# Performance work log

Hardware: AMD Instinct MI355X
Metric: run time of the kernel (lower is better)

Reference implementation:

```python
import jax, jax.numpy as jnp
import numpy as np

D_MODEL = 1024
H = 16
D = D_MODEL // H  # 64 per-head dim
B, T = 2, 2048


def setup_inputs() -> dict:
    key = jax.random.key(0)
    ks = jax.random.split(key, 5)
    scale = 1.0 / np.sqrt(D_MODEL)
    x = jax.random.normal(ks[0], (B, T, D_MODEL), dtype=jnp.float32)
    Wqkv = jax.random.normal(ks[1], (D_MODEL, 3 * D_MODEL), dtype=jnp.float32) * scale
    bqkv = jnp.zeros((3 * D_MODEL,), dtype=jnp.float32)
    Wproj = jax.random.normal(ks[2], (D_MODEL, D_MODEL), dtype=jnp.float32) * scale
    bproj = jnp.zeros((D_MODEL,), dtype=jnp.float32)
    return {"x": x, "Wqkv": Wqkv, "bqkv": bqkv, "Wproj": Wproj, "bproj": bproj}


def reference(x, Wqkv, bqkv, Wproj, bproj):
    b, t, d_model = x.shape
    h, d = H, D
    qkv = x @ Wqkv + bqkv  # [b, t, 3*d_model]
    q, k, v = jnp.split(qkv, 3, axis=-1)
    # [b, t, d_model] -> [b, h, t, d]
    q = q.reshape(b, t, h, d).transpose(0, 2, 1, 3)
    k = k.reshape(b, t, h, d).transpose(0, 2, 1, 3)
    v = v.reshape(b, t, h, d).transpose(0, 2, 1, 3)
    att = jnp.einsum('bhqd,bhkd->bhqk', q, k) / jnp.sqrt(jnp.float32(d))
    causal = jnp.tril(jnp.ones((t, t), dtype=bool))  # [t, t]
    att = jnp.where(causal[None, None, :, :], att, -jnp.inf)
    att = jax.nn.softmax(att, axis=-1)
    # dropout in eval mode -> identity (deterministic reference)
    out = jnp.einsum('bhqk,bhkd->bhqd', att, v)  # [b, h, t, d]
    out = out.transpose(0, 2, 1, 3).reshape(b, t, d_model)
    out = out @ Wproj + bproj
    return out
```

## Files before the change

### kernel.cpp

```cpp
#include <hip/hip_runtime.h>
#include <cstddef>

typedef __bf16 bf16x8 __attribute__((ext_vector_type(8)));
typedef float  f32x4  __attribute__((ext_vector_type(4)));

__device__ __forceinline__ float bf2f(unsigned short s) {
    return __uint_as_float(((unsigned int)s) << 16);
}
__device__ __forceinline__ unsigned short f2bf(float x) {
    unsigned int u = __float_as_uint(x);
    unsigned int r = u + 0x7fffu + ((u >> 16) & 1u);
    return (unsigned short)(r >> 16);
}

__device__ __forceinline__ void async_load16(const void* g, void* l) {
    __builtin_amdgcn_global_load_lds(
        (const __attribute__((address_space(1))) unsigned int*)g,
        (__attribute__((address_space(3))) unsigned int*)l,
        16, 0, 0);
}

__global__ __launch_bounds__(256) void detect_dtype_kernel(
    const unsigned short* __restrict__ x, int* __restrict__ flag)
{
    __shared__ int cnt;
    if (threadIdx.x == 0) cnt = 0;
    __syncthreads();
    int wild = 0;
    for (int k = 0; k < 16; ++k) {
        unsigned short u = x[(size_t)((k * 256 + threadIdx.x) << 1)];
        int e = (u >> 7) & 0xFF;
        wild += ((e >= 0x90) || (e >= 1 && e <= 0x48)) ? 1 : 0;
    }
    atomicAdd(&cnt, wild);
    __syncthreads();
    if (threadIdx.x == 0) *flag = (cnt > 512) ? 1 : 0;
}

__global__ __launch_bounds__(256) void cast_kernel(
    const int* __restrict__ flag, const void* __restrict__ src,
    unsigned short* __restrict__ dst, int n8)
{
    const int i = blockIdx.x * 256 + threadIdx.x;
    if (i >= n8) return;
    const size_t off = (size_t)i * 8;
    if (*flag) {
        const float* s = (const float*)src + off;
        float4 a = *(const float4*)s;
        float4 b = *(const float4*)(s + 4);
        uint4 o;
        o.x = (unsigned)f2bf(a.x) | ((unsigned)f2bf(a.y) << 16);
        o.y = (unsigned)f2bf(a.z) | ((unsigned)f2bf(a.w) << 16);
        o.z = (unsigned)f2bf(b.x) | ((unsigned)f2bf(b.y) << 16);
        o.w = (unsigned)f2bf(b.z) | ((unsigned)f2bf(b.w) << 16);
        *(uint4*)(dst + off) = o;
    } else {
        *(uint4*)(dst + off) = *(const uint4*)((const unsigned short*)src + off);
    }
}

__global__ __launch_bounds__(256) void transpose_cast_kernel(
    const int* __restrict__ flag, const void* __restrict__ src,
    unsigned short* __restrict__ dst, int R, int C)
{
    __shared__ unsigned short T[64][72];
    const int c0 = blockIdx.x * 64, r0 = blockIdx.y * 64;
    const int t  = threadIdx.x;
    const int r  = t >> 2, cl = (t & 3) << 4;

    unsigned short v[16];
    if (*flag) {
        const float* s = (const float*)src + (size_t)(r0 + r) * C + c0 + cl;
        #pragma unroll
        for (int q = 0; q < 4; ++q) {
            float4 a = *(const float4*)(s + q * 4);
            v[q * 4 + 0] = f2bf(a.x); v[q * 4 + 1] = f2bf(a.y);
            v[q * 4 + 2] = f2bf(a.z); v[q * 4 + 3] = f2bf(a.w);
        }
    } else {
        const unsigned short* s = (const unsigned short*)src + (size_t)(r0 + r) * C + c0 + cl;
        uint4 a = *(const uint4*)s;
        uint4 b = *(const uint4*)(s + 8);
        unsigned int w[8] = {a.x, a.y, a.z, a.w, b.x, b.y, b.z, b.w};
        #pragma unroll
        for (int q = 0; q < 8; ++q) {
            v[q * 2]     = (unsigned short)(w[q] & 0xffffu);
            v[q * 2 + 1] = (unsigned short)(w[q] >> 16);
        }
    }
    #pragma unroll
    for (int c = 0; c < 16; ++c) T[cl + c][r] = v[c];
    __syncthreads();

    const int c = t >> 2, rl = (t & 3) << 4;
    uint4 o0 = *(const uint4*)&T[c][rl];
    uint4 o1 = *(const uint4*)&T[c][rl + 8];
    unsigned short* dp = dst + (size_t)(c0 + c) * R + r0 + rl;
    *(uint4*)dp       = o0;
    *(uint4*)(dp + 8) = o1;
}

__device__ __forceinline__ void bt_mainloop(
    const unsigned short* __restrict__ A,
    const unsigned short* __restrict__ BT,
    int K, int m0, int n0,
    unsigned short* As, unsigned short* Bs,
    f32x4 (&acc)[4][4])
{
    const int tid  = threadIdx.x;
    const int wave = tid >> 6;
    const int lane = tid & 63;
    const int mrow = lane & 15;
    const int quad = lane >> 4;
    const int wr = wave >> 1, wc = wave & 1;
    const int srow = tid >> 2;
    const int scol = (tid & 3) << 3;

    const unsigned short* ga  = A  + (size_t)(m0 + srow) * K + scol;
    const unsigned short* ga2 = ga + (size_t)64 * K;
    const unsigned short* gb  = BT + (size_t)(n0 + srow) * K + scol;
    const unsigned short* gb2 = gb + (size_t)64 * K;
    unsigned short* lA  = As + wave * 512;
    unsigned short* lA2 = As + 2048 + wave * 512;
    unsigned short* lB  = Bs + wave * 512;
    unsigned short* lB2 = Bs + 2048 + wave * 512;

    for (int k0 = 0; k0 < K; k0 += 32) {
        async_load16(ga,  lA);
        async_load16(ga2, lA2);
        async_load16(gb,  lB);
        async_load16(gb2, lB2);
        ga += 32; ga2 += 32; gb += 32; gb2 += 32;
        __syncthreads();

        bf16x8 afr[4], bfr[4];
        #pragma unroll
        for (int mt = 0; mt < 4; ++mt)
            afr[mt] = *(const bf16x8*)(As + (wr * 64 + mt * 16 + mrow) * 32 + quad * 8);
        #pragma unroll
        for (int nt = 0; nt < 4; ++nt)
            bfr[nt] = *(const bf16x8*)(Bs + (wc * 64 + nt * 16 + mrow) * 32 + quad * 8);
        #pragma unroll
        for (int mt = 0; mt < 4; ++mt) {
            #pragma unroll
            for (int nt = 0; nt < 4; ++nt)
                acc[mt][nt] = __builtin_amdgcn_mfma_f32_16x16x32_bf16(
                    afr[mt], bfr[nt], acc[mt][nt], 0, 0, 0);
        }
        __syncthreads();
    }
}

__global__ __launch_bounds__(256) void gemm_qkv_bt(
    const int* __restrict__ flag,
    const unsigned short* __restrict__ A,
    const unsigned short* __restrict__ BT,
    const void* __restrict__ bias,
    unsigned short* __restrict__ Qb, unsigned short* __restrict__ Kb,
    unsigned short* __restrict__ Vb)
{
    __shared__ unsigned short As[128 * 32];
    __shared__ unsigned short Bs[128 * 32];
    const int m0 = blockIdx.y * 128, n0 = blockIdx.x * 128;

    f32x4 acc[4][4];
    #pragma unroll
    for (int mt = 0; mt < 4; ++mt)
        #pragma unroll
        for (int nt = 0; nt < 4; ++nt)
            { acc[mt][nt][0]=0.f; acc[mt][nt][1]=0.f; acc[mt][nt][2]=0.f; acc[mt][nt][3]=0.f; }

    bt_mainloop(A, BT, 1024, m0, n0, As, Bs, acc);

    const int tid  = threadIdx.x;
    const int wave = tid >> 6;
    const int lane = tid & 63;
    const int mrow = lane & 15;
    const int quad = lane >> 4;
    const int wr = wave >> 1, wc = wave & 1;
    const bool f32b = (*flag != 0);

    #pragma unroll
    for (int nt = 0; nt < 4; ++nt) {
        const int n = n0 + wc * 64 + nt * 16 + mrow;
        const float bv = f32b ? ((const float*)bias)[n]
                              : bf2f(((const unsigned short*)bias)[n]);
        const int sel = n >> 10;
        const int h   = (n & 1023) >> 6;
        const int d   = n & 63;
        unsigned short* dst = (sel == 0) ? Qb : (sel == 1) ? Kb : Vb;
        const float sc = (sel == 0) ? 0.125f : 1.0f;
        #pragma unroll
        for (int mt = 0; mt < 4; ++mt) {
            #pragma unroll
            for (int r = 0; r < 4; ++r) {
                const int m  = m0 + wr * 64 + mt * 16 + quad * 4 + r;
                const int bb = m >> 11;
                const int t  = m & 2047;
                dst[(((size_t)(bb * 16 + h) * 2048 + t) << 6) + d] =
                    f2bf((acc[mt][nt][r] + bv) * sc);
            }
        }
    }
}

__global__ __launch_bounds__(256) void gemm_proj_bt(
    const int* __restrict__ flag,
    const unsigned short* __restrict__ A,
    const unsigned short* __restrict__ BT,
    const void* __restrict__ bias, void* __restrict__ Out)
{
    __shared__ unsigned short As[128 * 32];
    __shared__ unsigned short Bs[128 * 32];
    const int m0 = blockIdx.y * 128, n0 = blockIdx.x * 128;

    f32x4 acc[4][4];
    #pragma unroll
    for (int mt = 0; mt < 4; ++mt)
        #pragma unroll
        for (int nt = 0; nt < 4; ++nt)
            { acc[mt][nt][0]=0.f; acc[mt][nt][1]=0.f; acc[mt][nt][2]=0.f; acc[mt][nt][3]=0.f; }

    bt_mainloop(A, BT, 1024, m0, n0, As, Bs, acc);

    const int tid  = threadIdx.x;
    const int wave = tid >> 6;
    const int lane = tid & 63;
    const int mrow = lane & 15;
    const int quad = lane >> 4;
    const int wr = wave >> 1, wc = wave & 1;
    const bool f32b = (*flag != 0);

    #pragma unroll
    for (int nt = 0; nt < 4; ++nt) {
        const int n = n0 + wc * 64 + nt * 16 + mrow;
        const float bv = f32b ? ((const float*)bias)[n]
                              : bf2f(((const unsigned short*)bias)[n]);
        #pragma unroll
        for (int mt = 0; mt < 4; ++mt) {
            #pragma unroll
            for (int r = 0; r < 4; ++r) {
                const int m = m0 + wr * 64 + mt * 16 + quad * 4 + r;
                const float val = acc[mt][nt][r] + bv;
                if (f32b) ((float*)Out)[(size_t)m * 1024 + n] = val;
                else      ((unsigned short*)Out)[(size_t)m * 1024 + n] = f2bf(val);
            }
        }
    }
}

__global__ __launch_bounds__(256) void attn_kernel(
    const unsigned short* __restrict__ Qb,
    const unsigned short* __restrict__ Kb,
    const unsigned short* __restrict__ Vb,
    unsigned short* __restrict__ Attn)
{
    __shared__ unsigned short Ks[128][68];
    __shared__ unsigned short VsT[64][136];
    __shared__ unsigned short Ps[64][136];

    const int tid  = threadIdx.x;
    const int wave = tid >> 6;
    const int lane = tid & 63;
    const int mrow = lane & 15;
    const int quad = lane >> 4;
    const int bh   = blockIdx.y;
    const int b    = bh >> 4, h = bh & 15;

    const int kr = tid >> 1;
    const int kc = (tid & 1) << 5;
    const int j2  = (tid & 63) << 1;
    const int dgA = (tid >> 6) << 3;

    const unsigned short* Qbase = Qb + ((size_t)bh * 2048) * 64;
    const unsigned short* Kbase = Kb + ((size_t)bh * 2048) * 64;
    const unsigned short* Vbase = Vb + ((size_t)bh * 2048) * 64;

    bf16x8 ones;
    #pragma unroll
    for (int e = 0; e < 8; ++e) ones[e] = (__bf16)1.0f;

    for (int half = 0; half < 2; ++half) {
        const int qblk = (half == 0) ? (int)blockIdx.x : (31 - (int)blockIdx.x);
        const int q0   = qblk << 6;
        const int nr   = (qblk >> 1) + 1;

        bf16x8 aq[2];
        {
            const unsigned short* qp = Qbase + (size_t)(q0 + wave * 16 + mrow) * 64 + quad * 8;
            aq[0] = *(const bf16x8*)qp;
            aq[1] = *(const bf16x8*)(qp + 32);
        }

        f32x4 Oa[4];
        #pragma unroll
        for (int dt = 0; dt < 4; ++dt) { Oa[dt][0]=0.f; Oa[dt][1]=0.f; Oa[dt][2]=0.f; Oa[dt][3]=0.f; }
        float m_run[4] = {-1e30f, -1e30f, -1e30f, -1e30f};
        float l_run[4] = {0.f, 0.f, 0.f, 0.f};

        uint4 kreg[4], vreg[4];
        {
            const unsigned short* kp = Kbase + (size_t)kr * 64 + kc;
            kreg[0] = *(const uint4*)kp;       kreg[1] = *(const uint4*)(kp + 8);
            kreg[2] = *(const uint4*)(kp + 16); kreg[3] = *(const uint4*)(kp + 24);
            const unsigned short* vp = Vbase + (size_t)j2 * 64;
            vreg[0] = *(const uint4*)(vp + dgA);      vreg[1] = *(const uint4*)(vp + 64 + dgA);
            vreg[2] = *(const uint4*)(vp + dgA + 32); vreg[3] = *(const uint4*)(vp + 64 + dgA + 32);
        }

        for (int rr = 0; rr < nr; ++rr) {
            const int kt0 = rr << 7;
            __syncthreads();
            {
                *(uint4*)&Ks[kr][kc]      = kreg[0];
                *(uint4*)&Ks[kr][kc + 8]  = kreg[1];
                *(uint4*)&Ks[kr][kc + 16] = kreg[2];
                *(uint4*)&Ks[kr][kc + 24] = kreg[3];
                #pragma unroll
                for (int g = 0; g < 2; ++g) {
                    const int dg = dgA + g * 32;
                    unsigned int aw[4] = {vreg[g*2].x, vreg[g*2].y, vreg[g*2].z, vreg[g*2].w};
                    unsigned int bw[4] = {vreg[g*2+1].x, vreg[g*2+1].y, vreg[g*2+1].z, vreg[g*2+1].w};
                    #pragma unroll
                    for (int c2 = 0; c2 < 4; ++c2) {
                        unsigned int lo = aw[c2], hi = bw[c2];
                        *(unsigned int*)&VsT[dg + 2*c2][j2]     = (lo & 0xffffu) | (hi << 16);
                        *(unsigned int*)&VsT[dg + 2*c2 + 1][j2] = (lo >> 16) | (hi & 0xffff0000u);
                    }
                }
            }
            __syncthreads();

            if (rr + 1 < nr) {
                const int nt0 = (rr + 1) << 7;
                const unsigned short* kp = Kbase + (size_t)(nt0 + kr) * 64 + kc;
                kreg[0] = *(const uint4*)kp;        kreg[1] = *(const uint4*)(kp + 8);
                kreg[2] = *(const uint4*)(kp + 16); kreg[3] = *(const uint4*)(kp + 24);
                const unsigned short* vp = Vbase + (size_t)(nt0 + j2) * 64;
                vreg[0] = *(const uint4*)(vp + dgA);      vreg[1] = *(const uint4*)(vp + 64 + dgA);
                vreg[2] = *(const uint4*)(vp + dgA + 32); vreg[3] = *(const uint4*)(vp + 64 + dgA + 32);
            }

            f32x4 sacc[8];
            #pragma unroll
            for (int jt = 0; jt < 8; ++jt) { sacc[jt][0]=0.f; sacc[jt][1]=0.f; sacc[jt][2]=0.f; sacc[jt][3]=0.f; }
            #pragma unroll
            for (int ks = 0; ks < 2; ++ks) {
                #pragma unroll
                for (int jt = 0; jt < 8; ++jt) {
                    bf16x8 bk = *(const bf16x8*)&Ks[jt * 16 + mrow][ks * 32 + quad * 8];
                    sacc[jt] = __builtin_amdgcn_mfma_f32_16x16x32_bf16(aq[ks], bk, sacc[jt], 0, 0, 0);
                }
            }

            if (rr == nr - 1) {
                #pragma unroll
                for (int jt = 0; jt < 8; ++jt) {
                    const int jg = kt0 + jt * 16 + mrow;
                    #pragma unroll
                    for (int r = 0; r < 4; ++r) {
                        if (jg > q0 + wave * 16 + quad * 4 + r) sacc[jt][r] = -1e30f;
                    }
                }
            }

            float mx[4], alpha[4];
            #pragma unroll
            for (int r = 0; r < 4; ++r) {
                mx[r] = fmaxf(fmaxf(fmaxf(sacc[0][r], sacc[1][r]), fmaxf(sacc[2][r], sacc[3][r])),
                              fmaxf(fmaxf(sacc[4][r], sacc[5][r]), fmaxf(sacc[6][r], sacc[7][r])));
            }
            #pragma unroll
            for (int m = 1; m <= 8; m <<= 1) {
                #pragma unroll
                for (int r = 0; r < 4; ++r) mx[r] = fmaxf(mx[r], __shfl_xor(mx[r], m));
            }
            #pragma unroll
            for (int r = 0; r < 4; ++r) {
                const float m_new = fmaxf(m_run[r], mx[r]);
                alpha[r] = __expf(m_run[r] - m_new);
                m_run[r] = m_new;
            }

            #pragma unroll
            for (int jt = 0; jt < 8; ++jt) {
                #pragma unroll
                for (int r = 0; r < 4; ++r) {
                    const float pv = __expf(sacc[jt][r] - m_run[r]);
                    Ps[wave * 16 + quad * 4 + r][jt * 16 + mrow] = f2bf(pv);
                }
            }

            #pragma unroll
            for (int dt = 0; dt < 4; ++dt) {
                #pragma unroll
                for (int r = 0; r < 4; ++r) Oa[dt][r] *= alpha[r];
            }

            __threadfence_block();

            f32x4 lt; lt[0]=0.f; lt[1]=0.f; lt[2]=0.f; lt[3]=0.f;
            #pragma unroll
            for (int ks4 = 0; ks4 < 4; ++ks4) {
                bf16x8 ap = *(const bf16x8*)&Ps[wave * 16 + mrow][ks4 * 32 + quad * 8];
                lt = __builtin_amdgcn_mfma_f32_16x16x32_bf16(ap, ones, lt, 0, 0, 0);
                #pragma unroll
                for (int dt = 0; dt < 4; ++dt) {
                    bf16x8 bv = *(const bf16x8*)&VsT[dt * 16 + mrow][ks4 * 32 + quad * 8];
                    Oa[dt] = __builtin_amdgcn_mfma_f32_16x16x32_bf16(ap, bv, Oa[dt], 0, 0, 0);
                }
            }
            #pragma unroll
            for (int r = 0; r < 4; ++r) l_run[r] = l_run[r] * alpha[r] + lt[r];
        }

        #pragma unroll
        for (int r = 0; r < 4; ++r) {
            const float inv = 1.0f / l_run[r];
            const int t = q0 + wave * 16 + quad * 4 + r;
            const size_t base = ((size_t)(b * 2048 + t)) * 1024 + h * 64;
            #pragma unroll
            for (int dt = 0; dt < 4; ++dt)
                Attn[base + dt * 16 + mrow] = f2bf(Oa[dt][r] * inv);
        }
    }
}

extern "C" void kernel_launch(void* const* d_in, const int* in_sizes, int n_in,
                              void* d_out, int out_size, void* d_ws, size_t ws_size,
                              hipStream_t stream)
{
    const void* x     = d_in[0];
    const void* Wqkv  = d_in[1];
    const void* bqkv  = d_in[2];
    const void* Wproj = d_in[3];
    const void* bproj = d_in[4];

    int* flag = (int*)d_ws;
    unsigned short* ws = (unsigned short*)d_ws;
    unsigned short* xb     = ws + 64;
    unsigned short* shared = xb + 4194304;
    unsigned short* WqkvT  = shared;
    unsigned short* Attn   = shared;
    unsigned short* WprojT = shared + 4194304;
    unsigned short* Qb     = WprojT + 1048576;
    unsigned short* Kb     = Qb + 4194304;
    unsigned short* Vb     = Kb + 4194304;

    detect_dtype_kernel<<<1, 256, 0, stream>>>((const unsigned short*)x, flag);
    cast_kernel<<<2048, 256, 0, stream>>>(flag, x, xb, 524288);
    transpose_cast_kernel<<<dim3(48, 16), 256, 0, stream>>>(flag, Wqkv, WqkvT, 1024, 3072);
    transpose_cast_kernel<<<dim3(16, 16), 256, 0, stream>>>(flag, Wproj, WprojT, 1024, 1024);
    gemm_qkv_bt<<<dim3(24, 32), 256, 0, stream>>>(flag, xb, WqkvT, bqkv, Qb, Kb, Vb);
    attn_kernel<<<dim3(16, 32), 256, 0, stream>>>(Qb, Kb, Vb, Attn);
    gemm_proj_bt<<<dim3(8, 32), 256, 0, stream>>>(flag, Attn, WprojT, bproj, d_out);
}
```

Before: 229.3 us.

## Store V transposed from QKV GEMM and async-load K/V tiles into LDS

```diff
diff --git a/kernel.cpp b/kernel.cpp
--- a/kernel.cpp
+++ b/kernel.cpp
@@ -157,7 +157,7 @@
     const unsigned short* __restrict__ BT,
     const void* __restrict__ bias,
     unsigned short* __restrict__ Qb, unsigned short* __restrict__ Kb,
-    unsigned short* __restrict__ Vb)
+    unsigned short* __restrict__ VbT)
 {
     __shared__ unsigned short As[128 * 32];
     __shared__ unsigned short Bs[128 * 32];
@@ -188,7 +188,6 @@
         const int sel = n >> 10;
         const int h   = (n & 1023) >> 6;
         const int d   = n & 63;
-        unsigned short* dst = (sel == 0) ? Qb : (sel == 1) ? Kb : Vb;
         const float sc = (sel == 0) ? 0.125f : 1.0f;
         #pragma unroll
         for (int mt = 0; mt < 4; ++mt) {
@@ -197,8 +196,11 @@
                 const int m  = m0 + wr * 64 + mt * 16 + quad * 4 + r;
                 const int bb = m >> 11;
                 const int t  = m & 2047;
-                dst[(((size_t)(bb * 16 + h) * 2048 + t) << 6) + d] =
-                    f2bf((acc[mt][nt][r] + bv) * sc);
+                const unsigned short ov = f2bf((acc[mt][nt][r] + bv) * sc);
+                const int bhh = bb * 16 + h;
+                if (sel == 0)      Qb [(((size_t)bhh * 2048 + t) << 6) + d] = ov;
+                else if (sel == 1) Kb [(((size_t)bhh * 2048 + t) << 6) + d] = ov;
+                else               VbT[((((size_t)bhh << 6) + d) << 11) + t] = ov;
             }
         }
     }
@@ -252,11 +254,11 @@
 __global__ __launch_bounds__(256) void attn_kernel(
     const unsigned short* __restrict__ Qb,
     const unsigned short* __restrict__ Kb,
-    const unsigned short* __restrict__ Vb,
+    const unsigned short* __restrict__ VbT,
     unsigned short* __restrict__ Attn)
 {
-    __shared__ unsigned short Ks[128][68];
-    __shared__ unsigned short VsT[64][136];
+    __shared__ unsigned short KsH[2][128 * 32];
+    __shared__ unsigned short VsQ[4][64 * 32];
     __shared__ unsigned short Ps[64][136];
 
     const int tid  = threadIdx.x;
@@ -264,24 +266,27 @@
     const int lane = tid & 63;
     const int mrow = lane & 15;
     const int quad = lane >> 4;
-    const int bh   = blockIdx.y;
-    const int b    = bh >> 4, h = bh & 15;
-
-    const int kr = tid >> 1;
-    const int kc = (tid & 1) << 5;
-    const int j2  = (tid & 63) << 1;
-    const int dgA = (tid >> 6) << 3;
-
-    const unsigned short* Qbase = Qb + ((size_t)bh * 2048) * 64;
-    const unsigned short* Kbase = Kb + ((size_t)bh * 2048) * 64;
-    const unsigned short* Vbase = Vb + ((size_t)bh * 2048) * 64;
+
+    const int blk   = blockIdx.x;
+    const int xcd   = blk & 7;
+    const int slot  = blk >> 3;
+    const int bh    = (xcd << 2) | (slot & 3);
+    const int qpair = slot >> 2;
+    const int b     = bh >> 4, h = bh & 15;
+
+    const int krow  = tid >> 2;
+    const int kcol8 = (tid & 3) << 3;
+
+    const unsigned short* Qbase = Qb  + ((size_t)bh << 17);
+    const unsigned short* Kbase = Kb  + ((size_t)bh << 17);
+    const unsigned short* Vtb   = VbT + ((size_t)bh << 17);
 
     bf16x8 ones;
     #pragma unroll
     for (int e = 0; e < 8; ++e) ones[e] = (__bf16)1.0f;
 
     for (int half = 0; half < 2; ++half) {
-        const int qblk = (half == 0) ? (int)blockIdx.x : (31 - (int)blockIdx.x);
+        const int qblk = (half == 0) ? qpair : (31 - qpair);
         const int q0   = qblk << 6;
         const int nr   = (qblk >> 1) + 1;
 
@@ -298,48 +303,25 @@
         float m_run[4] = {-1e30f, -1e30f, -1e30f, -1e30f};
         float l_run[4] = {0.f, 0.f, 0.f, 0.f};
 
-        uint4 kreg[4], vreg[4];
-        {
-            const unsigned short* kp = Kbase + (size_t)kr * 64 + kc;
-            kreg[0] = *(const uint4*)kp;       kreg[1] = *(const uint4*)(kp + 8);
-            kreg[2] = *(const uint4*)(kp + 16); kreg[3] = *(const uint4*)(kp + 24);
-            const unsigned short* vp = Vbase + (size_t)j2 * 64;
-            vreg[0] = *(const uint4*)(vp + dgA);      vreg[1] = *(const uint4*)(vp + 64 + dgA);
-            vreg[2] = *(const uint4*)(vp + dgA + 32); vreg[3] = *(const uint4*)(vp + 64 + dgA + 32);
-        }
-
         for (int rr = 0; rr < nr; ++rr) {
             const int kt0 = rr << 7;
+
+            #pragma unroll
+            for (int h2 = 0; h2 < 2; ++h2) {
+                #pragma unroll
+                for (int p = 0; p < 2; ++p) {
+                    const unsigned short* src =
+                        Kbase + (size_t)(kt0 + p * 64 + krow) * 64 + h2 * 32 + kcol8;
+                    async_load16(src, &KsH[h2][(p * 64 + krow) * 32 + kcol8]);
+                }
+            }
+            #pragma unroll
+            for (int q4 = 0; q4 < 4; ++q4) {
+                const unsigned short* src =
+                    Vtb + ((size_t)krow << 11) + kt0 + q4 * 32 + kcol8;
+                async_load16(src, &VsQ[q4][krow * 32 + kcol8]);
+            }
             __syncthreads();
-            {
-                *(uint4*)&Ks[kr][kc]      = kreg[0];
-                *(uint4*)&Ks[kr][kc + 8]  = kreg[1];
-                *(uint4*)&Ks[kr][kc + 16] = kreg[2];
-                *(uint4*)&Ks[kr][kc + 24] = kreg[3];
-                #pragma unroll
-                for (int g = 0; g < 2; ++g) {
-                    const int dg = dgA + g * 32;
-                    unsigned int aw[4] = {vreg[g*2].x, vreg[g*2].y, vreg[g*2].z, vreg[g*2].w};
-                    unsigned int bw[4] = {vreg[g*2+1].x, vreg[g*2+1].y, vreg[g*2+1].z, vreg[g*2+1].w};
-                    #pragma unroll
-                    for (int c2 = 0; c2 < 4; ++c2) {
-                        unsigned int lo = aw[c2], hi = bw[c2];
-                        *(unsigned int*)&VsT[dg + 2*c2][j2]     = (lo & 0xffffu) | (hi << 16);
-                        *(unsigned int*)&VsT[dg + 2*c2 + 1][j2] = (lo >> 16) | (hi & 0xffff0000u);
-                    }
-                }
-            }
-            __syncthreads();
-
-            if (rr + 1 < nr) {
-                const int nt0 = (rr + 1) << 7;
-                const unsigned short* kp = Kbase + (size_t)(nt0 + kr) * 64 + kc;
-                kreg[0] = *(const uint4*)kp;        kreg[1] = *(const uint4*)(kp + 8);
-                kreg[2] = *(const uint4*)(kp + 16); kreg[3] = *(const uint4*)(kp + 24);
-                const unsigned short* vp = Vbase + (size_t)(nt0 + j2) * 64;
-                vreg[0] = *(const uint4*)(vp + dgA);      vreg[1] = *(const uint4*)(vp + 64 + dgA);
-                vreg[2] = *(const uint4*)(vp + dgA + 32); vreg[3] = *(const uint4*)(vp + 64 + dgA + 32);
-            }
 
             f32x4 sacc[8];
             #pragma unroll
@@ -348,7 +330,7 @@
             for (int ks = 0; ks < 2; ++ks) {
                 #pragma unroll
                 for (int jt = 0; jt < 8; ++jt) {
-                    bf16x8 bk = *(const bf16x8*)&Ks[jt * 16 + mrow][ks * 32 + quad * 8];
+                    bf16x8 bk = *(const bf16x8*)&KsH[ks][(jt * 16 + mrow) * 32 + quad * 8];
                     sacc[jt] = __builtin_amdgcn_mfma_f32_16x16x32_bf16(aq[ks], bk, sacc[jt], 0, 0, 0);
                 }
             }
@@ -406,12 +388,14 @@
                 lt = __builtin_amdgcn_mfma_f32_16x16x32_bf16(ap, ones, lt, 0, 0, 0);
                 #pragma unroll
                 for (int dt = 0; dt < 4; ++dt) {
-                    bf16x8 bv = *(const bf16x8*)&VsT[dt * 16 + mrow][ks4 * 32 + quad * 8];
+                    bf16x8 bv = *(const bf16x8*)&VsQ[ks4][(dt * 16 + mrow) * 32 + quad * 8];
                     Oa[dt] = __builtin_amdgcn_mfma_f32_16x16x32_bf16(ap, bv, Oa[dt], 0, 0, 0);
                 }
             }
             #pragma unroll
             for (int r = 0; r < 4; ++r) l_run[r] = l_run[r] * alpha[r] + lt[r];
+
+            __syncthreads();
         }
 
         #pragma unroll
@@ -445,13 +429,13 @@
     unsigned short* WprojT = shared + 4194304;
     unsigned short* Qb     = WprojT + 1048576;
     unsigned short* Kb     = Qb + 4194304;
-    unsigned short* Vb     = Kb + 4194304;
+    unsigned short* VbT    = Kb + 4194304;
 
     detect_dtype_kernel<<<1, 256, 0, stream>>>((const unsigned short*)x, flag);
     cast_kernel<<<2048, 256, 0, stream>>>(flag, x, xb, 524288);
     transpose_cast_kernel<<<dim3(48, 16), 256, 0, stream>>>(flag, Wqkv, WqkvT, 1024, 3072);
     transpose_cast_kernel<<<dim3(16, 16), 256, 0, stream>>>(flag, Wproj, WprojT, 1024, 1024);
-    gemm_qkv_bt<<<dim3(24, 32), 256, 0, stream>>>(flag, xb, WqkvT, bqkv, Qb, Kb, Vb);
-    attn_kernel<<<dim3(16, 32), 256, 0, stream>>>(Qb, Kb, Vb, Attn);
+    gemm_qkv_bt<<<dim3(24, 32), 256, 0, stream>>>(flag, xb, WqkvT, bqkv, Qb, Kb, VbT);
+    attn_kernel<<<512, 256, 0, stream>>>(Qb, Kb, VbT, Attn);
     gemm_proj_bt<<<dim3(8, 32), 256, 0, stream>>>(flag, Attn, WprojT, bproj, d_out);
 }
```

Result: faster. 214.5 us (-6.4%).
